# Kernel tuning notes

Measured on AMD Instinct MI355X. Metric: run time of the kernel, lower is better.

Reference implementation:

```python
import jax, jax.numpy as jnp
import numpy as np

SCALE = 0.5          # centroids_input_scale
MAX_STRIDE = 16      # centroids_max_stride
CM_STRIDE = 2        # centroids_confmaps_stride (backbone overall stride)
THRESH = 0.2         # peak_threshold
CROP = 160           # crop_size
K = 32               # max peaks per sample (ragged -> dense+mask)
PATCH = 5            # integral-refinement patch size (sleap default)


def setup_inputs() -> dict:
    key = jax.random.key(0)
    k1, k2, k3 = jax.random.split(key, 3)
    full_imgs = jax.random.uniform(k1, (16, 1024, 1024, 1), jnp.float32)
    w1 = jax.random.normal(k2, (5, 5, 1, 32), jnp.float32) * 0.1
    b1 = jnp.zeros((32,), jnp.float32)
    w2 = jax.random.normal(k3, (5, 5, 32, 1), jnp.float32) * 0.1
    b2 = jnp.zeros((1,), jnp.float32)
    return {"full_imgs": full_imgs, "w1": w1, "b1": b1, "w2": w2, "b2": b2}


def _conv(x, w, stride):
    return jax.lax.conv_general_dilated(
        x, w, (stride, stride), 'SAME',
        dimension_numbers=('NHWC', 'HWIO', 'NHWC'))


def _centroid_model(x, w1, b1, w2, b2):
    h = jax.nn.relu(_conv(x, w1, CM_STRIDE) + b1)
    return jax.nn.sigmoid(_conv(h, w2, 1) + b2)  # [B,Hc,Wc,1]


def _forward(full_imgs, w1, b1, w2, b2):
    B, H, W, C = full_imgs.shape
    # --- resize_image + pad_to_stride ---
    hs, ws = int(H * SCALE), int(W * SCALE)
    imgs = jax.image.resize(full_imgs, (B, hs, ws, C), 'bilinear')
    ph, pw = (-hs) % MAX_STRIDE, (-ws) % MAX_STRIDE
    imgs = jnp.pad(imgs, ((0, 0), (0, ph), (0, pw), (0, 0)))
    # --- centroid confmaps ---
    cms = _centroid_model(imgs, w1, b1, w2, b2)[..., 0]  # [B,Hc,Wc]
    Hc, Wc = cms.shape[1], cms.shape[2]
    # --- find_local_peaks: 3x3 NMS + threshold, top-K per sample ---
    mx = jax.lax.reduce_window(cms, -jnp.inf, jax.lax.max,
                               (1, 3, 3), (1, 1, 1), 'SAME')
    is_peak = (cms >= mx) & (cms > THRESH)
    scores = jnp.where(is_peak, cms, -jnp.inf).reshape(B, -1)
    vals, idx = jax.lax.top_k(scores, K)            # [B,K]
    valid = jnp.isfinite(vals)                      # [B,K] bool
    py = idx // Wc
    px = idx % Wc
    # --- integral refinement over PATCH x PATCH (zero outside bounds) ---
    off = jnp.arange(PATCH) - (PATCH - 1) // 2      # [-2..2]
    yy = py[..., None, None] + off[None, None, :, None]   # [B,K,P,P]
    xx = px[..., None, None] + off[None, None, None, :]
    inb = (yy >= 0) & (yy < Hc) & (xx >= 0) & (xx < Wc)
    yc = jnp.clip(yy, 0, Hc - 1)
    xc = jnp.clip(xx, 0, Wc - 1)
    bidx = jnp.arange(B)[:, None, None, None]
    patches = cms[bidx, yc, xc] * inb               # [B,K,P,P]
    gv = patches.sum((-2, -1)) + 1e-12
    fo = off.astype(cms.dtype)
    dx = (patches * fo[None, None, None, :]).sum((-2, -1)) / gv
    dy = (patches * fo[None, None, :, None]).sum((-2, -1)) / gv
    # --- map back to full-image coords ---
    cx = (px.astype(cms.dtype) + dx) * CM_STRIDE / SCALE
    cy = (py.astype(cms.dtype) + dy) * CM_STRIDE / SCALE
    cx = jnp.where(valid, cx, CROP / 2)
    cy = jnp.where(valid, cy, CROP / 2)
    centroid_vals = jnp.where(valid, vals, 0.0)
    crop_offsets = jnp.stack([cx - CROP / 2, cy - CROP / 2], axis=-1)  # (x,y)
    # --- crop_bboxes: bilinear crop of CROPxCROP, (CROP-1)-pixel span ---
    gi = jnp.arange(CROP, dtype=cms.dtype)
    sy = (cy - (CROP - 1) / 2)[..., None] + gi      # [B,K,CROP] row coords
    sx = (cx - (CROP - 1) / 2)[..., None] + gi      # [B,K,CROP] col coords
    y0 = jnp.floor(sy); x0 = jnp.floor(sx)
    wy = (sy - y0)[..., :, None, None]              # [B,K,CROP,1,1]
    wx = (sx - x0)[..., None, :, None]              # [B,K,1,CROP,1]
    yi0 = jnp.clip(y0.astype(jnp.int32), 0, H - 1)
    yi1 = jnp.clip(y0.astype(jnp.int32) + 1, 0, H - 1)
    xi0 = jnp.clip(x0.astype(jnp.int32), 0, W - 1)
    xi1 = jnp.clip(x0.astype(jnp.int32) + 1, 0, W - 1)

    def gath(yi, xi):  # -> [B,K,CROP,CROP,C]
        return full_imgs[bidx, yi[..., :, None], xi[..., None, :], :]

    top = gath(yi0, xi0) * (1 - wx) + gath(yi0, xi1) * wx
    bot = gath(yi1, xi0) * (1 - wx) + gath(yi1, xi1) * wx
    crops = top * (1 - wy) + bot * wy
    # crop_and_resize extrapolation_value=0 outside the image
    inr = (((sy >= 0) & (sy <= H - 1))[..., :, None]
           & ((sx >= 0) & (sx <= W - 1))[..., None, :])
    crops = crops * inr[..., None] * valid[..., None, None, None]
    return crops, crop_offsets, centroid_vals, valid


def reference(full_imgs, w1, b1, w2, b2):
    return _forward(full_imgs, w1, b1, w2, b2)
```

## Files before the change

kernel.cpp:

```cpp
#include <hip/hip_runtime.h>
#include <math.h>

#define BATCH 16
#define HF 1024
#define WF 1024
#define HS 512
#define WS2 512
#define HC 256
#define WC 256
#define KMAX 32
#define CAP 16384
#define CROPSZ 160
#define CNT_STRIDE 16
#define NCHUNK 16
#define CHUNK 1024

#define IMGP_W 524
#define IMGP_H 524
#define IMGP_STRIDE (IMGP_W * IMGP_H)

#define CMS_PLANE 1048576UL
#define THRESH_Z -1.38629436112f

#define OFF_IMGS 0UL
#define OFF_CMS  17572864UL
#define OFF_KEYS (OFF_CMS + 8388608UL)
#define OFF_CNT  (OFF_KEYS + 2097152UL)
#define OFF_CX   (OFF_CNT + 2048UL)
#define OFF_CY   (OFF_CX + 2048UL)
#define OFF_VLD  (OFF_CY + 2048UL)
#define OFF_CAND (OFF_VLD + 2048UL)

#define OUT_CROPS 0
#define OUT_OFFS  13107200
#define OUT_VALS  13108224
#define OUT_VALID 13108736

__global__ __launch_bounds__(256) void resize_kernel(const float* __restrict__ full,
                                                     float* __restrict__ imgs,
                                                     int* __restrict__ counts) {
    if (blockIdx.x == 0 && blockIdx.y == 0 && threadIdx.x < BATCH * CNT_STRIDE)
        counts[threadIdx.x] = 0;
    __shared__ float simg[10][1024];
    int tid = threadIdx.x;
    int y0 = blockIdx.x << 2;
    int b = blockIdx.y;
    const float* base = full + ((size_t)b << 20);
    float* ob = imgs + (size_t)b * IMGP_STRIDE;
    if (tid < 48) {
        int r = tid / 12, c = tid - (tid / 12) * 12;
        int col = c < 5 ? c : 512 + c;
        ob[(size_t)(5 + y0 + r) * IMGP_W + col] = 0.f;
    }
    if (blockIdx.x == 0)
        for (int i = tid; i < 5 * IMGP_W; i += 256) ob[i] = 0.f;
    if (blockIdx.x == 127)
        for (int i = tid; i < 7 * IMGP_W; i += 256)
            ob[(size_t)517 * IMGP_W + i] = 0.f;
#pragma unroll
    for (int s = 0; s < 10; ++s) {
        int r = 2 * y0 - 1 + s;
        r = r < 0 ? 0 : (r > HF - 1 ? HF - 1 : r);
        ((float4*)simg[s])[tid] = ((const float4*)(base + r * WF))[tid];
    }
    __syncthreads();
    const float w4[4] = {0.125f, 0.375f, 0.375f, 0.125f};
#pragma unroll
    for (int p = 0; p < 2; ++p) {
        int x = tid + 256 * p;
        float wx[4];
        int rx[4];
        float sx = 0.f;
#pragma unroll
        for (int ii = 0; ii < 4; ++ii) {
            int c = 2 * x - 1 + ii;
            float wc = (c >= 0 && c < WF) ? w4[ii] : 0.f;
            wx[ii] = wc; sx += wc;
            rx[ii] = c < 0 ? 0 : (c >= WF ? WF - 1 : c);
        }
#pragma unroll
        for (int r = 0; r < 4; ++r) {
            int yy = y0 + r;
            float sy = 0.f;
            float wy[4];
#pragma unroll
            for (int j = 0; j < 4; ++j) {
                int rr = 2 * yy - 1 + j;
                float w = (rr >= 0 && rr < HF) ? w4[j] : 0.f;
                wy[j] = w; sy += w;
            }
            float acc = 0.f;
#pragma unroll
            for (int j = 0; j < 4; ++j) {
                float rowacc = 0.f;
                const float* sr = simg[2 * r + j];
#pragma unroll
                for (int ii = 0; ii < 4; ++ii) rowacc += wx[ii] * sr[rx[ii]];
                acc += wy[j] * rowacc;
            }
            ob[(size_t)(5 + yy) * IMGP_W + 5 + x] = acc * (1.f / (sy * sx));
        }
    }
}

__global__ __launch_bounds__(256, 4) void conv_fused2_kernel(
    const float* __restrict__ imgs, const float* __restrict__ w1,
    const float* __restrict__ b1, const float* __restrict__ w2,
    const float* __restrict__ b2, float* __restrict__ cms) {
    __shared__ float4 sh[36][37];
    int tid = threadIdx.x;
    int b = blockIdx.y >> 1;
    int half = blockIdx.y & 1;
    int q0 = half << 2;
    int Y0 = (blockIdx.x >> 3) << 5;
    int X0 = (blockIdx.x & 7) << 5;
    const float* ib = imgs + (size_t)b * IMGP_STRIDE;

    bool c1act = tid < 216;
    int ghy = tid / 6;
    int ghx0 = (tid - ghy * 6) * 6;
    const float* gbase = ib + (size_t)(2 * Y0 + 2 * ghy) * IMGP_W
                            + (2 * X0 + 2 * ghx0);
    float4* shw = &sh[ghy][ghx0];
    bool rowok = (unsigned)(Y0 - 2 + ghy) < 256u;
    int gx0 = X0 - 2 + ghx0;

    int cx = tid & 31;
    int ry0 = (tid >> 5) << 2;
    const float4* hb = &sh[ry0][cx];
    float4 zv0 = make_float4(0.f, 0.f, 0.f, 0.f);
    float4 zv1 = zv0, zv2 = zv0, zv3 = zv0;

    for (int qi = 0; qi < 4; ++qi) {
        int q = q0 + qi;
        float4 wq[25];
        const float4* w14 = (const float4*)w1;
#pragma unroll
        for (int t = 0; t < 25; ++t) wq[t] = w14[t * 8 + q];
        float4 bq = ((const float4*)b1)[q];

        int qoff = 0;
        asm volatile("" : "+v"(qoff));
        const float* gb = gbase + qoff;

        __syncthreads();

        if (c1act) {
            float4 acc[6];
#pragma unroll
            for (int j = 0; j < 6; ++j) acc[j] = bq;
#pragma unroll
            for (int ky = 0; ky < 5; ++ky) {
                const float* rp = gb + ky * IMGP_W;
                float4 f0 = *(const float4*)(rp);
                float4 f1 = *(const float4*)(rp + 4);
                float4 f2 = *(const float4*)(rp + 8);
                float4 f3 = *(const float4*)(rp + 12);
                float f[16] = {f0.x, f0.y, f0.z, f0.w, f1.x, f1.y, f1.z, f1.w,
                               f2.x, f2.y, f2.z, f2.w, f3.x, f3.y, f3.z, f3.w};
#pragma unroll
                for (int j = 0; j < 6; ++j)
#pragma unroll
                    for (int kx = 0; kx < 5; ++kx) {
                        float v = f[2 * j + kx];
                        float4 w = wq[ky * 5 + kx];
                        acc[j].x += v * w.x; acc[j].y += v * w.y;
                        acc[j].z += v * w.z; acc[j].w += v * w.w;
                    }
            }
#pragma unroll
            for (int j = 0; j < 6; ++j) {
                float4 r;
                bool ok = rowok && ((unsigned)(gx0 + j) < 256u);
                r.x = ok ? fmaxf(acc[j].x, 0.f) : 0.f;
                r.y = ok ? fmaxf(acc[j].y, 0.f) : 0.f;
                r.z = ok ? fmaxf(acc[j].z, 0.f) : 0.f;
                r.w = ok ? fmaxf(acc[j].w, 0.f) : 0.f;
                shw[j] = r;
            }
        }

        const float4* w24 = (const float4*)w2;
#pragma unroll
        for (int t = 0; t < 25; ++t) wq[t] = w24[t * 8 + q];

        __syncthreads();

#pragma unroll
        for (int rr = 0; rr < 8; ++rr) {
#pragma unroll
            for (int kx = 0; kx < 5; ++kx) {
                float4 hv = hb[rr * 37 + kx];
#pragma unroll
                for (int j = 0; j < 4; ++j) {
                    int ky = rr - j;
                    if (ky < 0 || ky > 4) continue;
                    float4 w = wq[ky * 5 + kx];
                    if (j == 0) {
                        zv0.x += hv.x * w.x; zv0.y += hv.y * w.y;
                        zv0.z += hv.z * w.z; zv0.w += hv.w * w.w;
                    } else if (j == 1) {
                        zv1.x += hv.x * w.x; zv1.y += hv.y * w.y;
                        zv1.z += hv.z * w.z; zv1.w += hv.w * w.w;
                    } else if (j == 2) {
                        zv2.x += hv.x * w.x; zv2.y += hv.y * w.y;
                        zv2.z += hv.z * w.z; zv2.w += hv.w * w.w;
                    } else {
                        zv3.x += hv.x * w.x; zv3.y += hv.y * w.y;
                        zv3.z += hv.z * w.z; zv3.w += hv.w * w.w;
                    }
                }
            }
        }
    }

    float bb = half ? 0.f : b2[0];
    float z0 = bb + zv0.x + zv0.y + zv0.z + zv0.w;
    float z1 = bb + zv1.x + zv1.y + zv1.z + zv1.w;
    float z2 = bb + zv2.x + zv2.y + zv2.z + zv2.w;
    float z3 = bb + zv3.x + zv3.y + zv3.z + zv3.w;
    size_t ob = (size_t)half * CMS_PLANE + ((size_t)b << 16)
              + ((size_t)(Y0 + ry0) << 8) + (X0 + cx);
    cms[ob]       = z0;
    cms[ob + 256] = z1;
    cms[ob + 512] = z2;
    cms[ob + 768] = z3;
}

__global__ __launch_bounds__(256) void peak_scan_kernel(
    const float* __restrict__ cms, unsigned long long* __restrict__ keys,
    int* __restrict__ counts) {
    int bidx = blockIdx.x;
    int b = bidx >> 6;
    int y0 = (bidx & 63) << 2;
    int x = threadIdx.x;
    const float* pa = cms + ((size_t)b << 16);
    const float* pb = cms + CMS_PLANE + ((size_t)b << 16);
    __shared__ float rows[6][256];
    __shared__ int lcnt, lbase;
    if (x == 0) lcnt = 0;
#pragma unroll
    for (int j = 0; j < 6; ++j) {
        int yy = y0 - 1 + j;
        rows[j][x] = (yy >= 0 && yy < HC)
                         ? pa[yy * WC + x] + pb[yy * WC + x] : -INFINITY;
    }
    __syncthreads();
    int pidx[4];
    unsigned long long pkey[4];
#pragma unroll
    for (int r = 0; r < 4; ++r) {
        float c = rows[r + 1][x];
        bool peak = (c > THRESH_Z);
        if (peak) {
#pragma unroll
            for (int j = 0; j < 3; ++j) {
                const float* rw = rows[r + j];
                float r0 = rw[x];
                float rl = (x > 0)   ? rw[x - 1] : -INFINITY;
                float rr = (x < 255) ? rw[x + 1] : -INFINITY;
                if (fmaxf(r0, fmaxf(rl, rr)) > c) peak = false;
            }
        }
        pidx[r] = -1;
        if (peak) {
            pidx[r] = atomicAdd(&lcnt, 1);
            unsigned u = __float_as_uint(c);
            u = (u & 0x80000000u) ? ~u : (u | 0x80000000u);
            int i = (y0 + r) * WC + x;
            pkey[r] = ((unsigned long long)u << 32) |
                      (unsigned long long)(0xFFFFFFFFu - (unsigned)i);
        }
    }
    __syncthreads();
    if (x == 0) lbase = lcnt ? atomicAdd(&counts[b * CNT_STRIDE], lcnt) : 0;
    __syncthreads();
#pragma unroll
    for (int r = 0; r < 4; ++r)
        if (pidx[r] >= 0) {
            int pos = lbase + pidx[r];
            if (pos < CAP) keys[(size_t)b * CAP + pos] = pkey[r];
        }
}

__global__ __launch_bounds__(64) void topk_stage_a(
    const unsigned long long* __restrict__ keys, const int* __restrict__ counts,
    unsigned long long* __restrict__ cand) {
    int b = blockIdx.x >> 4;
    int chunk = blockIdx.x & 15;
    int lane = threadIdx.x;
    int cnt = counts[b * CNT_STRIDE]; if (cnt > CAP) cnt = CAP;
    const unsigned long long* kb = keys + (size_t)b * CAP + chunk * CHUNK;
    int lim = cnt - chunk * CHUNK;
    unsigned long long v[16];
#pragma unroll
    for (int j = 0; j < 16; ++j) {
        int i = lane + (j << 6);
        v[j] = (i < lim) ? kb[i] : 0ULL;
    }
    unsigned long long* out = cand + (size_t)(b * NCHUNK + chunk) * KMAX;
    int k = 0;
    for (; k < KMAX; ++k) {
        unsigned long long best = v[0];
#pragma unroll
        for (int j = 1; j < 16; ++j) best = v[j] > best ? v[j] : best;
#pragma unroll
        for (int s = 1; s < 64; s <<= 1) {
            unsigned long long o = __shfl_xor(best, s, 64);
            if (o > best) best = o;
        }
        if (best == 0ULL) break;
        if (lane == 0) out[k] = best;
#pragma unroll
        for (int j = 0; j < 16; ++j) if (v[j] == best) v[j] = 0ULL;
    }
    if (lane >= k && lane < KMAX) out[lane] = 0ULL;
}

__global__ __launch_bounds__(64) void topk_stage_b(
    const float* __restrict__ cms, const unsigned long long* __restrict__ cand,
    float* __restrict__ out_off, float* __restrict__ out_vals,
    float* __restrict__ out_valid, float* __restrict__ ws_cx,
    float* __restrict__ ws_cy, float* __restrict__ ws_v) {
    int b = blockIdx.x;
    int lane = threadIdx.x;
    unsigned long long v[8];
#pragma unroll
    for (int j = 0; j < 8; ++j)
        v[j] = cand[(size_t)b * 512 + lane + (j << 6)];
    unsigned long long mysel = 0ULL;
    for (int k = 0; k < KMAX; ++k) {
        unsigned long long best = v[0];
#pragma unroll
        for (int j = 1; j < 8; ++j) best = v[j] > best ? v[j] : best;
#pragma unroll
        for (int s = 1; s < 64; s <<= 1) {
            unsigned long long o = __shfl_xor(best, s, 64);
            if (o > best) best = o;
        }
        if (best == 0ULL) break;
        if (lane == k) mysel = best;
#pragma unroll
        for (int j = 0; j < 8; ++j) if (v[j] == best) v[j] = 0ULL;
    }
    if (lane < KMAX) {
        unsigned long long key = mysel;
        bool valid = key != 0ULL;
        float cx = 80.f, cy = 80.f, val = 0.f;
        if (valid) {
            unsigned f = (unsigned)(key >> 32);
            unsigned u = (f & 0x80000000u) ? (f & 0x7FFFFFFFu) : ~f;
            float z = __uint_as_float(u);
            val = 1.f / (1.f + expf(-z));
            int idx = (int)(0xFFFFFFFFu - (unsigned)(key & 0xFFFFFFFFULL));
            int py = idx >> 8, px = idx & 255;
            const float* pa = cms + ((size_t)b << 16);
            const float* pb = cms + CMS_PLANE + ((size_t)b << 16);
            float gv = 1e-12f, sdx = 0.f, sdy = 0.f;
#pragma unroll
            for (int oy = -2; oy <= 2; ++oy)
#pragma unroll
                for (int ox = -2; ox <= 2; ++ox) {
                    int yy = py + oy, xx = px + ox;
                    if (yy < 0 || yy >= HC || xx < 0 || xx >= WC) continue;
                    float zz = pa[yy * WC + xx] + pb[yy * WC + xx];
                    float pv = 1.f / (1.f + expf(-zz));
                    gv += pv; sdx += pv * (float)ox; sdy += pv * (float)oy;
                }
            float dx = sdx / gv, dy = sdy / gv;
            cx = ((float)px + dx) * 4.f;
            cy = ((float)py + dy) * 4.f;
        }
        int o = b * KMAX + lane;
        out_off[o * 2 + 0] = cx - 80.f;
        out_off[o * 2 + 1] = cy - 80.f;
        out_vals[o] = val;
        out_valid[o] = valid ? 1.f : 0.f;
        ws_cx[o] = cx; ws_cy[o] = cy; ws_v[o] = valid ? 1.f : 0.f;
    }
}

__global__ __launch_bounds__(256) void crop_kernel(
    const float* __restrict__ full, const float* __restrict__ ws_cx,
    const float* __restrict__ ws_cy, const float* __restrict__ ws_v,
    float* __restrict__ out_crops) {
    int bidx = blockIdx.x;
    int cid = bidx / 25;
    int p = (bidx - cid * 25) * 256 + threadIdx.x;
    int b = cid >> 5;
    float cx = ws_cx[cid], cy = ws_cy[cid], v = ws_v[cid];
    int rg = p / CROPSZ;
    int col = p - rg * CROPSZ;
    int r0 = rg << 2;
    float sx = cx - 79.5f + (float)col;
    float x0f = floorf(sx);
    float wx = sx - x0f;
    int x0 = (int)x0f;
    int xi0 = min(max(x0, 0), WF - 1);
    int xi1 = min(max(x0 + 1, 0), WF - 1);
    float syb = cy - 79.5f + (float)r0;
    float y0f = floorf(syb);
    float wy = syb - y0f;
    int y0 = (int)y0f;
    const float* base = full + ((size_t)b << 20);
    float rv[5];
#pragma unroll
    for (int i = 0; i < 5; ++i) {
        int yy = min(max(y0 + i, 0), HF - 1);
        float a = base[yy * WF + xi0];
        float c = base[yy * WF + xi1];
        rv[i] = a * (1.f - wx) + c * wx;
    }
    bool xin = (sx >= 0.f && sx <= (float)(WF - 1));
    size_t ob = (size_t)cid * (CROPSZ * CROPSZ) + r0 * CROPSZ + col;
#pragma unroll
    for (int i = 0; i < 4; ++i) {
        float sy = syb + (float)i;
        float val = rv[i] * (1.f - wy) + rv[i + 1] * wy;
        float inr = (xin && sy >= 0.f && sy <= (float)(HF - 1)) ? 1.f : 0.f;
        out_crops[ob + i * CROPSZ] = val * inr * v;
    }
}

extern "C" void kernel_launch(void* const* d_in, const int* in_sizes, int n_in,
                              void* d_out, int out_size, void* d_ws, size_t ws_size,
                              hipStream_t stream) {
    const float* full = (const float*)d_in[0];
    const float* w1   = (const float*)d_in[1];
    const float* b1   = (const float*)d_in[2];
    const float* w2   = (const float*)d_in[3];
    const float* b2   = (const float*)d_in[4];

    char* ws = (char*)d_ws;
    float* imgs = (float*)(ws + OFF_IMGS);
    float* cms  = (float*)(ws + OFF_CMS);
    unsigned long long* keys = (unsigned long long*)(ws + OFF_KEYS);
    int* counts = (int*)(ws + OFF_CNT);
    float* ws_cx = (float*)(ws + OFF_CX);
    float* ws_cy = (float*)(ws + OFF_CY);
    float* ws_v  = (float*)(ws + OFF_VLD);
    unsigned long long* cand = (unsigned long long*)(ws + OFF_CAND);

    float* out = (float*)d_out;
    float* out_crops = out + OUT_CROPS;
    float* out_off   = out + OUT_OFFS;
    float* out_vals  = out + OUT_VALS;
    float* out_valid = out + OUT_VALID;

    hipLaunchKernelGGL(resize_kernel, dim3(128, 16), dim3(256), 0, stream,
                       full, imgs, counts);

    hipLaunchKernelGGL(conv_fused2_kernel, dim3(64, 32), dim3(256), 0, stream,
                       imgs, w1, b1, w2, b2, cms);

    hipLaunchKernelGGL(peak_scan_kernel, dim3(1024), dim3(256), 0, stream,
                       cms, keys, counts);
    hipLaunchKernelGGL(topk_stage_a, dim3(256), dim3(64), 0, stream,
                       keys, counts, cand);
    hipLaunchKernelGGL(topk_stage_b, dim3(16), dim3(64), 0, stream,
                       cms, cand, out_off, out_vals, out_valid,
                       ws_cx, ws_cy, ws_v);
    hipLaunchKernelGGL(crop_kernel, dim3(12800), dim3(256), 0, stream,
                       full, ws_cx, ws_cy, ws_v, out_crops);
}
```

Measured before the change: 251.5 us.

## Fuse peak scan and two-stage top-k into one kernel with last-block finish

Merges the peak scan, per-chunk top-k and final top-k/refinement kernels into a single kernel. Each block scans a 16-row strip, keeps its peaks in a shared-memory list, reduces them to a local top-32 and writes that to global memory. The last block to finish for each sample, detected with an atomic counter and fences, then runs the final merge. This removes two launches and the global keys round trip, but caps each block's candidate list at 2048 entries and relies on the counter being zeroed by the resize kernel.

```diff
diff --git a/kernel.cpp b/kernel.cpp
--- a/kernel.cpp
+++ b/kernel.cpp
@@ -14,6 +14,7 @@
 #define CNT_STRIDE 16
 #define NCHUNK 16
 #define CHUNK 1024
+#define LISTCAP 2048
 
 #define IMGP_W 524
 #define IMGP_H 524
@@ -227,123 +228,140 @@
     cms[ob + 768] = z3;
 }
 
-__global__ __launch_bounds__(256) void peak_scan_kernel(
-    const float* __restrict__ cms, unsigned long long* __restrict__ keys,
-    int* __restrict__ counts) {
-    int bidx = blockIdx.x;
-    int b = bidx >> 6;
-    int y0 = (bidx & 63) << 2;
-    int x = threadIdx.x;
-    const float* pa = cms + ((size_t)b << 16);
-    const float* pb = cms + CMS_PLANE + ((size_t)b << 16);
-    __shared__ float rows[6][256];
-    __shared__ int lcnt, lbase;
-    if (x == 0) lcnt = 0;
-#pragma unroll
-    for (int j = 0; j < 6; ++j) {
-        int yy = y0 - 1 + j;
-        rows[j][x] = (yy >= 0 && yy < HC)
-                         ? pa[yy * WC + x] + pb[yy * WC + x] : -INFINITY;
-    }
-    __syncthreads();
-    int pidx[4];
-    unsigned long long pkey[4];
-#pragma unroll
-    for (int r = 0; r < 4; ++r) {
-        float c = rows[r + 1][x];
-        bool peak = (c > THRESH_Z);
-        if (peak) {
-#pragma unroll
-            for (int j = 0; j < 3; ++j) {
-                const float* rw = rows[r + j];
-                float r0 = rw[x];
-                float rl = (x > 0)   ? rw[x - 1] : -INFINITY;
-                float rr = (x < 255) ? rw[x + 1] : -INFINITY;
-                if (fmaxf(r0, fmaxf(rl, rr)) > c) peak = false;
-            }
-        }
-        pidx[r] = -1;
-        if (peak) {
-            pidx[r] = atomicAdd(&lcnt, 1);
-            unsigned u = __float_as_uint(c);
-            u = (u & 0x80000000u) ? ~u : (u | 0x80000000u);
-            int i = (y0 + r) * WC + x;
-            pkey[r] = ((unsigned long long)u << 32) |
-                      (unsigned long long)(0xFFFFFFFFu - (unsigned)i);
-        }
-    }
-    __syncthreads();
-    if (x == 0) lbase = lcnt ? atomicAdd(&counts[b * CNT_STRIDE], lcnt) : 0;
-    __syncthreads();
-#pragma unroll
-    for (int r = 0; r < 4; ++r)
-        if (pidx[r] >= 0) {
-            int pos = lbase + pidx[r];
-            if (pos < CAP) keys[(size_t)b * CAP + pos] = pkey[r];
-        }
-}
-
-__global__ __launch_bounds__(64) void topk_stage_a(
-    const unsigned long long* __restrict__ keys, const int* __restrict__ counts,
-    unsigned long long* __restrict__ cand) {
-    int b = blockIdx.x >> 4;
-    int chunk = blockIdx.x & 15;
-    int lane = threadIdx.x;
-    int cnt = counts[b * CNT_STRIDE]; if (cnt > CAP) cnt = CAP;
-    const unsigned long long* kb = keys + (size_t)b * CAP + chunk * CHUNK;
-    int lim = cnt - chunk * CHUNK;
-    unsigned long long v[16];
-#pragma unroll
-    for (int j = 0; j < 16; ++j) {
-        int i = lane + (j << 6);
-        v[j] = (i < lim) ? kb[i] : 0ULL;
-    }
-    unsigned long long* out = cand + (size_t)(b * NCHUNK + chunk) * KMAX;
-    int k = 0;
-    for (; k < KMAX; ++k) {
-        unsigned long long best = v[0];
-#pragma unroll
-        for (int j = 1; j < 16; ++j) best = v[j] > best ? v[j] : best;
-#pragma unroll
-        for (int s = 1; s < 64; s <<= 1) {
-            unsigned long long o = __shfl_xor(best, s, 64);
-            if (o > best) best = o;
-        }
-        if (best == 0ULL) break;
-        if (lane == 0) out[k] = best;
-#pragma unroll
-        for (int j = 0; j < 16; ++j) if (v[j] == best) v[j] = 0ULL;
-    }
-    if (lane >= k && lane < KMAX) out[lane] = 0ULL;
-}
-
-__global__ __launch_bounds__(64) void topk_stage_b(
-    const float* __restrict__ cms, const unsigned long long* __restrict__ cand,
+__global__ __launch_bounds__(256) void peak_topk_kernel(
+    const float* __restrict__ cms, int* __restrict__ done,
+    unsigned long long* __restrict__ cand,
     float* __restrict__ out_off, float* __restrict__ out_vals,
     float* __restrict__ out_valid, float* __restrict__ ws_cx,
     float* __restrict__ ws_cy, float* __restrict__ ws_v) {
-    int b = blockIdx.x;
-    int lane = threadIdx.x;
+    int bidx = blockIdx.x;
+    int b = bidx >> 4;
+    int s = bidx & 15;
+    int y0 = s << 4;
+    int tid = threadIdx.x;
+    int lane = tid & 63;
+    int wv = tid >> 6;
+    __shared__ float zs[18][264];
+    __shared__ unsigned long long list[LISTCAP];
+    __shared__ unsigned long long wtop[4][KMAX];
+    __shared__ int lcnt;
+    __shared__ int flag;
+    if (tid == 0) { lcnt = 0; flag = 0; }
+    if (tid < 36) {
+        int r = tid >> 1;
+        zs[r][(tid & 1) ? 3 : 260] = -INFINITY;
+    }
+    const float* pa = cms + ((size_t)b << 16);
+    const float* pb = cms + CMS_PLANE + ((size_t)b << 16);
+    for (int i = tid; i < 18 * 64; i += 256) {
+        int r = i >> 6;
+        int c4 = i & 63;
+        int yy = y0 - 1 + r;
+        float4 v4 = make_float4(-INFINITY, -INFINITY, -INFINITY, -INFINITY);
+        if ((unsigned)yy < 256u) {
+            float4 a  = ((const float4*)(pa + ((size_t)yy << 8)))[c4];
+            float4 bv = ((const float4*)(pb + ((size_t)yy << 8)))[c4];
+            v4 = make_float4(a.x + bv.x, a.y + bv.y, a.z + bv.z, a.w + bv.w);
+        }
+        ((float4*)&zs[r][4])[c4] = v4;
+    }
+    __syncthreads();
+    {
+        int x = tid;
+        float m0 = fmaxf(fmaxf(zs[0][3 + x], zs[0][4 + x]), zs[0][5 + x]);
+        float m1 = fmaxf(fmaxf(zs[1][3 + x], zs[1][4 + x]), zs[1][5 + x]);
+#pragma unroll
+        for (int r = 0; r < 16; ++r) {
+            float m2 = fmaxf(fmaxf(zs[r + 2][3 + x], zs[r + 2][4 + x]),
+                             zs[r + 2][5 + x]);
+            float c = zs[r + 1][4 + x];
+            bool peak = (c > THRESH_Z) && (c >= m0) && (c >= m1) && (c >= m2);
+            if (peak) {
+                int pos = atomicAdd(&lcnt, 1);
+                if (pos < LISTCAP) {
+                    unsigned u = __float_as_uint(c);
+                    u = (u & 0x80000000u) ? ~u : (u | 0x80000000u);
+                    int idx = (y0 + r) * WC + x;
+                    list[pos] = ((unsigned long long)u << 32) |
+                                (unsigned long long)(0xFFFFFFFFu - (unsigned)idx);
+                }
+            }
+            m0 = m1; m1 = m2;
+        }
+    }
+    __syncthreads();
+    int n = lcnt; if (n > LISTCAP) n = LISTCAP;
     unsigned long long v[8];
 #pragma unroll
+    for (int j = 0; j < 8; ++j) {
+        int i = tid + (j << 8);
+        v[j] = (i < n) ? list[i] : 0ULL;
+    }
+    int kw = 0;
+    for (; kw < KMAX; ++kw) {
+        unsigned long long best = v[0];
+#pragma unroll
+        for (int j = 1; j < 8; ++j) best = v[j] > best ? v[j] : best;
+#pragma unroll
+        for (int st = 1; st < 64; st <<= 1) {
+            unsigned long long o = __shfl_xor(best, st, 64);
+            if (o > best) best = o;
+        }
+        if (best == 0ULL) break;
+        if (lane == 0) wtop[wv][kw] = best;
+#pragma unroll
+        for (int j = 0; j < 8; ++j) if (v[j] == best) v[j] = 0ULL;
+    }
+    if (lane >= kw && lane < KMAX) wtop[wv][lane] = 0ULL;
+    __syncthreads();
+    unsigned long long* ob = cand + (size_t)(b * NCHUNK + s) * KMAX;
+    if (wv == 0) {
+        unsigned long long u0 = ((unsigned long long*)wtop)[lane];
+        unsigned long long u1 = ((unsigned long long*)wtop)[lane + 64];
+        int k = 0;
+        for (; k < KMAX; ++k) {
+            unsigned long long best = u0 > u1 ? u0 : u1;
+#pragma unroll
+            for (int st = 1; st < 64; st <<= 1) {
+                unsigned long long o = __shfl_xor(best, st, 64);
+                if (o > best) best = o;
+            }
+            if (best == 0ULL) break;
+            if (lane == 0) ob[k] = best;
+            if (u0 == best) u0 = 0ULL;
+            if (u1 == best) u1 = 0ULL;
+        }
+        if (lane >= k && lane < KMAX) ob[lane] = 0ULL;
+    }
+    __syncthreads();
+    if (tid == 0) {
+        __threadfence();
+        int old = atomicAdd(&done[b * CNT_STRIDE], 1);
+        flag = (old == 15) ? 1 : 0;
+    }
+    __syncthreads();
+    if (!flag || tid >= 64) return;
+    __threadfence();
+    unsigned long long vb[8];
+#pragma unroll
     for (int j = 0; j < 8; ++j)
-        v[j] = cand[(size_t)b * 512 + lane + (j << 6)];
+        vb[j] = cand[(size_t)b * 512 + tid + (j << 6)];
     unsigned long long mysel = 0ULL;
     for (int k = 0; k < KMAX; ++k) {
-        unsigned long long best = v[0];
-#pragma unroll
-        for (int j = 1; j < 8; ++j) best = v[j] > best ? v[j] : best;
-#pragma unroll
-        for (int s = 1; s < 64; s <<= 1) {
-            unsigned long long o = __shfl_xor(best, s, 64);
+        unsigned long long best = vb[0];
+#pragma unroll
+        for (int j = 1; j < 8; ++j) best = vb[j] > best ? vb[j] : best;
+#pragma unroll
+        for (int st = 1; st < 64; st <<= 1) {
+            unsigned long long o = __shfl_xor(best, st, 64);
             if (o > best) best = o;
         }
         if (best == 0ULL) break;
-        if (lane == k) mysel = best;
-#pragma unroll
-        for (int j = 0; j < 8; ++j) if (v[j] == best) v[j] = 0ULL;
-    }
-    if (lane < KMAX) {
+        if (tid == k) mysel = best;
+#pragma unroll
+        for (int j = 0; j < 8; ++j) if (vb[j] == best) vb[j] = 0ULL;
+    }
+    if (tid < KMAX) {
         unsigned long long key = mysel;
         bool valid = key != 0ULL;
         float cx = 80.f, cy = 80.f, val = 0.f;
@@ -354,8 +372,6 @@
             val = 1.f / (1.f + expf(-z));
             int idx = (int)(0xFFFFFFFFu - (unsigned)(key & 0xFFFFFFFFULL));
             int py = idx >> 8, px = idx & 255;
-            const float* pa = cms + ((size_t)b << 16);
-            const float* pb = cms + CMS_PLANE + ((size_t)b << 16);
             float gv = 1e-12f, sdx = 0.f, sdy = 0.f;
 #pragma unroll
             for (int oy = -2; oy <= 2; ++oy)
@@ -371,7 +387,7 @@
             cx = ((float)px + dx) * 4.f;
             cy = ((float)py + dy) * 4.f;
         }
-        int o = b * KMAX + lane;
+        int o = b * KMAX + tid;
         out_off[o * 2 + 0] = cx - 80.f;
         out_off[o * 2 + 1] = cy - 80.f;
         out_vals[o] = val;
@@ -434,7 +450,6 @@
     char* ws = (char*)d_ws;
     float* imgs = (float*)(ws + OFF_IMGS);
     float* cms  = (float*)(ws + OFF_CMS);
-    unsigned long long* keys = (unsigned long long*)(ws + OFF_KEYS);
     int* counts = (int*)(ws + OFF_CNT);
     float* ws_cx = (float*)(ws + OFF_CX);
     float* ws_cy = (float*)(ws + OFF_CY);
@@ -453,13 +468,10 @@
     hipLaunchKernelGGL(conv_fused2_kernel, dim3(64, 32), dim3(256), 0, stream,
                        imgs, w1, b1, w2, b2, cms);
 
-    hipLaunchKernelGGL(peak_scan_kernel, dim3(1024), dim3(256), 0, stream,
-                       cms, keys, counts);
-    hipLaunchKernelGGL(topk_stage_a, dim3(256), dim3(64), 0, stream,
-                       keys, counts, cand);
-    hipLaunchKernelGGL(topk_stage_b, dim3(16), dim3(64), 0, stream,
-                       cms, cand, out_off, out_vals, out_valid,
+    hipLaunchKernelGGL(peak_topk_kernel, dim3(256), dim3(256), 0, stream,
+                       cms, counts, cand, out_off, out_vals, out_valid,
                        ws_cx, ws_cy, ws_v);
+
     hipLaunchKernelGGL(crop_kernel, dim3(12800), dim3(256), 0, stream,
                        full, ws_cx, ws_cy, ws_v, out_crops);
 }
```

Result: slower. 258.0 us (+2.6%).
